# Performance work log

Hardware: AMD Instinct MI355X
Metric: run time of the kernel (lower is better)

The kernel has to match this reference:

```python
import jax, jax.numpy as jnp
from jax import lax
import numpy as np

N_ITER = 50  # entmax.EntmaxBisect default n_iter


def _p(z, alpha):
    # inverse of g'(t) = t**(alpha-1): clamp then fractional power
    return jnp.maximum(z, 0.0) ** (1.0 / (alpha - 1.0))


def entmax_bisect(x, alpha):
    """alpha-entmax over the last axis via 50-step bisection (entmax.EntmaxBisect)."""
    am1 = alpha - 1.0
    X = x * am1
    d = X.shape[-1]
    max_val = jnp.max(X, axis=-1, keepdims=True)
    tau_lo = max_val - 1.0                    # max - _gp(1, alpha)
    tau_hi = max_val - (1.0 / d) ** am1       # max - _gp(1/d, alpha)
    f_lo = jnp.sum(_p(X - tau_lo, alpha), axis=-1, keepdims=True) - 1.0
    dm0 = tau_hi - tau_lo

    def body(i, carry):
        dm, tlo, _ = carry
        dm = dm / 2.0
        tau_m = tlo + dm
        p_m = _p(X - tau_m, alpha)
        f_m = jnp.sum(p_m, axis=-1, keepdims=True) - 1.0
        mask = (f_m * f_lo) >= 0.0
        tlo = jnp.where(mask, tau_m, tlo)
        return dm, tlo, p_m

    _, _, p_m = lax.fori_loop(0, N_ITER, body, (dm0, tau_lo, jnp.zeros_like(X)))
    # ensure_sum_one=True
    return p_m / jnp.sum(p_m, axis=-1, keepdims=True)


def setup_inputs() -> dict:
    key = jax.random.key(0)
    in_value = jax.random.normal(key, (2048, 32000), dtype=jnp.float32)
    alpha = jnp.asarray(1.5, dtype=jnp.float32)  # the q parameter
    return {"in_value": in_value, "alpha": alpha}


def reference(in_value, alpha):
    return entmax_bisect(in_value, alpha)
```

## Files before the change

### kernel.cpp

```cpp
#include <hip/hip_runtime.h>
#include <math.h>


#define D_DIM   32000
#define NV4     (D_DIM / 4)
#define BLOCK   512
#define NWAVE   (BLOCK / 64)
#define NCHUNK  16
#define CAP     6144
#define NEWTON_MAX 30
#define NITER   50

__device__ __forceinline__ float wave_sum(float v) {
#pragma unroll
    for (int off = 32; off > 0; off >>= 1) v += __shfl_xor(v, off, 64);
    return v;
}
__device__ __forceinline__ float wave_max(float v) {
#pragma unroll
    for (int off = 32; off > 0; off >>= 1) v = fmaxf(v, __shfl_xor(v, off, 64));
    return v;
}
__device__ __forceinline__ float pf(float z, bool sq, float expo) {
    z = fmaxf(z, 0.0f);
    return sq ? z * z : powf(z, expo);
}
__device__ __forceinline__ unsigned fflip(float f) {
    unsigned u = __float_as_uint(f);
    return u ^ ((u >> 31) ? 0xFFFFFFFFu : 0x80000000u);
}
__device__ __forceinline__ float funflip(unsigned u) {
    return __uint_as_float(u ^ ((u & 0x80000000u) ? 0x80000000u : 0xFFFFFFFFu));
}

__global__ __launch_bounds__(BLOCK, 2)
void entmax_bisect_kernel(const float* __restrict__ x,
                          const float* __restrict__ alpha_p,
                          float* __restrict__ out) {
    const int row  = blockIdx.x;
    const int tid  = threadIdx.x;
    const int lane = tid & 63;
    const int wid  = tid >> 6;

    __shared__ float          s_val[CAP];
    __shared__ unsigned short s_idx[CAP];
    __shared__ float          s_red[NWAVE];
    __shared__ float          s_bc[2];
    __shared__ int            s_cnt;
    __shared__ unsigned       s_gmax;

    const float alpha   = alpha_p[0];
    const float am1     = alpha - 1.0f;
    const float inv_am1 = 1.0f / am1;
    const float expo    = inv_am1;
    const bool  sq      = (expo == 2.0f);

    const float4* __restrict__ x4 = (const float4*)(x + (size_t)row * D_DIM);
    float4*       __restrict__ o4 = (float4*)(out + (size_t)row * D_DIM);

    if (tid == 0) { s_cnt = 0; s_gmax = 0u; }
    __syncthreads();

    const float4 zero4 = make_float4(0.f, 0.f, 0.f, 0.f);
    float4 v[NCHUNK];
#pragma unroll
    for (int k = 0; k < NCHUNK; ++k) {
        const int i4 = tid + (k << 9);
        if (i4 < NV4) v[k] = x4[i4];
        else          v[k] = make_float4(-INFINITY, -INFINITY, -INFINITY, -INFINITY);
    }
    __builtin_amdgcn_sched_barrier(0);
#pragma unroll
    for (int k = 0; k < NCHUNK; ++k) {
        const int i4 = tid + (k << 9);
        if (i4 < NV4) o4[i4] = zero4;
    }
    __builtin_amdgcn_sched_barrier(0);

    float tm = -INFINITY;
#pragma unroll
    for (int k = 0; k < NCHUNK; ++k)
        tm = fmaxf(tm, fmaxf(fmaxf(v[k].x, v[k].y), fmaxf(v[k].z, v[k].w)));
    const float wm  = wave_max(tm);
    const float wmX = wm * am1;
    if (lane == 0) atomicMax(&s_gmax, fflip(wmX));
    const unsigned r = __hip_atomic_load(&s_gmax, __ATOMIC_RELAXED,
                                         __HIP_MEMORY_SCOPE_WORKGROUP);
    const float run   = fmaxf(funflip(r), wmX);
    const float thr_x = (run - 1.0f) * inv_am1;

    int cnt = 0;
#pragma unroll
    for (int k = 0; k < NCHUNK; ++k) {
        cnt += (v[k].x > thr_x) + (v[k].y > thr_x)
             + (v[k].z > thr_x) + (v[k].w > thr_x);
    }
    int inc = cnt;
#pragma unroll
    for (int off = 1; off < 64; off <<= 1) {
        const int t = __shfl_up(inc, off, 64);
        if (lane >= off) inc += t;
    }
    const int total = __shfl(inc, 63, 64);
    if (total > 0) {
        int base = 0;
        if (lane == 63) base = atomicAdd(&s_cnt, total);
        base = __shfl(base, 63, 64);
        int pos = base + (inc - cnt);
        auto append1 = [&](float val, int idx) {
            if (val > thr_x) {
                if (pos < CAP) {
                    s_val[pos] = val * am1;
                    s_idx[pos] = (unsigned short)idx;
                }
                ++pos;
            }
        };
#pragma unroll
        for (int k = 0; k < NCHUNK; ++k) {
            const int e = (tid << 2) + k * 2048;
            append1(v[k].x, e);     append1(v[k].y, e + 1);
            append1(v[k].z, e + 2); append1(v[k].w, e + 3);
        }
    }
    __syncthreads();
    const int   n_act   = s_cnt;
    const float max_val = funflip(s_gmax);
    const float tau_lo0 = max_val - 1.0f;

    if (n_act <= CAP) {
        if (wid == 0) {
            float tau, S;
            if (sq) {
                tau = tau_lo0;
                for (int it = 0; it < NEWTON_MAX; ++it) {
                    float s1 = 0.f, s2 = 0.f;
                    for (int i = lane; i < n_act; i += 64) {
                        const float z = fmaxf(s_val[i] - tau, 0.f);
                        s1 += z; s2 += z * z;
                    }
#pragma unroll
                    for (int off = 32; off > 0; off >>= 1) {
                        s1 += __shfl_xor(s1, off, 64);
                        s2 += __shfl_xor(s2, off, 64);
                    }
                    const float dtau = (s2 - 1.0f) / fmaxf(2.0f * s1, 1e-30f);
                    tau += dtau;
                    if (dtau < 1e-7f * fmaxf(1.0f, fabsf(tau))) break;
                }
                float s2 = 0.f;
                for (int i = lane; i < n_act; i += 64) {
                    const float z = fmaxf(s_val[i] - tau, 0.f);
                    s2 += z * z;
                }
                S = wave_sum(s2);
            } else {
                const float tau_hi = max_val - powf(1.0f / (float)D_DIM, am1);
                float dm = tau_hi - tau_lo0;
                float s = 0.f;
                for (int i = lane; i < n_act; i += 64)
                    s += pf(s_val[i] - tau_lo0, sq, expo);
                s = wave_sum(s);
                const float f_lo = s - 1.0f;
                float tlo = tau_lo0, tau_m = tau_lo0, fsum = s;
                for (int it = 0; it < NITER; ++it) {
                    dm *= 0.5f;
                    tau_m = tlo + dm;
                    float t = 0.f;
                    for (int i = lane; i < n_act; i += 64)
                        t += pf(s_val[i] - tau_m, sq, expo);
                    t = wave_sum(t);
                    fsum = t;
                    if ((t - 1.0f) * f_lo >= 0.0f) tlo = tau_m;
                }
                tau = tau_m; S = fsum;
            }
            if (lane == 0) { s_bc[0] = tau; s_bc[1] = S; }
        }
        __syncthreads();

        const float tau_f = s_bc[0];
        const float invS  = 1.0f / s_bc[1];
        for (int i = tid; i < n_act; i += BLOCK) {
            const float z = fmaxf(s_val[i] - tau_f, 0.f);
            const float p = sq ? z * z : powf(z, expo);
            out[(size_t)row * D_DIM + s_idx[i]] = p * invS;
        }
    } else {
        const float tau_hi = max_val - powf(1.0f / (float)D_DIM, am1);
        float dm = tau_hi - tau_lo0;
        float s = 0.f;
        for (int i4 = tid; i4 < NV4; i4 += BLOCK) {
            float4 vv = x4[i4];
            s += pf(vv.x * am1 - tau_lo0, sq, expo) + pf(vv.y * am1 - tau_lo0, sq, expo)
               + pf(vv.z * am1 - tau_lo0, sq, expo) + pf(vv.w * am1 - tau_lo0, sq, expo);
        }
        s = wave_sum(s);
        __syncthreads();
        if (lane == 0) s_red[wid] = s;
        __syncthreads();
        float tot = 0.f;
#pragma unroll
        for (int w = 0; w < NWAVE; ++w) tot += s_red[w];
        const float f_lo = tot - 1.0f;
        float tlo = tau_lo0, tau_m = tau_lo0, fsum = tot;
        for (int it = 0; it < NITER; ++it) {
            dm *= 0.5f;
            tau_m = tlo + dm;
            float t = 0.f;
            for (int i4 = tid; i4 < NV4; i4 += BLOCK) {
                float4 vv = x4[i4];
                t += pf(vv.x * am1 - tau_m, sq, expo) + pf(vv.y * am1 - tau_m, sq, expo)
                   + pf(vv.z * am1 - tau_m, sq, expo) + pf(vv.w * am1 - tau_m, sq, expo);
            }
            t = wave_sum(t);
            __syncthreads();
            if (lane == 0) s_red[wid] = t;
            __syncthreads();
            float tt = 0.f;
#pragma unroll
            for (int w = 0; w < NWAVE; ++w) tt += s_red[w];
            fsum = tt;
            if ((tt - 1.0f) * f_lo >= 0.0f) tlo = tau_m;
        }
        const float invS = 1.0f / fsum;
        __syncthreads();
        for (int i4 = tid; i4 < NV4; i4 += BLOCK) {
            float4 vv = x4[i4];
            float4 o;
            o.x = pf(vv.x * am1 - tau_m, sq, expo) * invS;
            o.y = pf(vv.y * am1 - tau_m, sq, expo) * invS;
            o.z = pf(vv.z * am1 - tau_m, sq, expo) * invS;
            o.w = pf(vv.w * am1 - tau_m, sq, expo) * invS;
            o4[i4] = o;
        }
    }
}

extern "C" void kernel_launch(void* const* d_in, const int* in_sizes, int n_in,
                              void* d_out, int out_size, void* d_ws, size_t ws_size,
                              hipStream_t stream) {
    const float* x       = (const float*)d_in[0];
    const float* alpha_p = (const float*)d_in[1];
    float* out           = (float*)d_out;
    const int rows       = in_sizes[0] / D_DIM;
    entmax_bisect_kernel<<<rows, BLOCK, 0, stream>>>(x, alpha_p, out);
}
```

Before: 470.5 us.

## Write dense output from registers instead of zero-fill plus sparse scatter

```diff
diff --git a/kernel.cpp b/kernel.cpp
--- a/kernel.cpp
+++ b/kernel.cpp
@@ -11,6 +11,8 @@
 #define NEWTON_MAX 30
 #define NITER   50
 
+typedef float f32x4 __attribute__((ext_vector_type(4)));
+
 __device__ __forceinline__ float wave_sum(float v) {
 #pragma unroll
     for (int off = 32; off > 0; off >>= 1) v += __shfl_xor(v, off, 64);
@@ -42,12 +44,11 @@
     const int lane = tid & 63;
     const int wid  = tid >> 6;
 
-    __shared__ float          s_val[CAP];
-    __shared__ unsigned short s_idx[CAP];
-    __shared__ float          s_red[NWAVE];
-    __shared__ float          s_bc[2];
-    __shared__ int            s_cnt;
-    __shared__ unsigned       s_gmax;
+    __shared__ float    s_val[CAP];
+    __shared__ float    s_red[NWAVE];
+    __shared__ float    s_bc[2];
+    __shared__ int      s_cnt;
+    __shared__ unsigned s_gmax;
 
     const float alpha   = alpha_p[0];
     const float am1     = alpha - 1.0f;
@@ -55,32 +56,33 @@
     const float expo    = inv_am1;
     const bool  sq      = (expo == 2.0f);
 
-    const float4* __restrict__ x4 = (const float4*)(x + (size_t)row * D_DIM);
-    float4*       __restrict__ o4 = (float4*)(out + (size_t)row * D_DIM);
+    const float* __restrict__ rowp = x + (size_t)row * D_DIM;
+    const float4* __restrict__ x4  = (const float4*)rowp;
+    float4*       __restrict__ o4  = (float4*)(out + (size_t)row * D_DIM);
 
     if (tid == 0) { s_cnt = 0; s_gmax = 0u; }
     __syncthreads();
 
-    const float4 zero4 = make_float4(0.f, 0.f, 0.f, 0.f);
-    float4 v[NCHUNK];
+    f32x4 v[NCHUNK];
 #pragma unroll
     for (int k = 0; k < NCHUNK; ++k) {
-        const int i4 = tid + (k << 9);
-        if (i4 < NV4) v[k] = x4[i4];
-        else          v[k] = make_float4(-INFINITY, -INFINITY, -INFINITY, -INFINITY);
-    }
+        const int i4   = tid + (k << 9);
+        const int safe = (i4 < NV4) ? i4 : (NV4 - 1);
+        const unsigned boff = (unsigned)safe * 16u;
+        asm volatile("global_load_dwordx4 %0, %1, %2"
+                     : "=v"(v[k]) : "v"(boff), "s"(rowp));
+    }
+    asm volatile("s_waitcnt vmcnt(0)" ::: "memory");
     __builtin_amdgcn_sched_barrier(0);
 #pragma unroll
-    for (int k = 0; k < NCHUNK; ++k) {
-        const int i4 = tid + (k << 9);
-        if (i4 < NV4) o4[i4] = zero4;
-    }
-    __builtin_amdgcn_sched_barrier(0);
+    for (int k = 0; k < NCHUNK; ++k)
+        if (tid + (k << 9) >= NV4)
+            v[k] = (f32x4){-INFINITY, -INFINITY, -INFINITY, -INFINITY};
 
     float tm = -INFINITY;
 #pragma unroll
     for (int k = 0; k < NCHUNK; ++k)
-        tm = fmaxf(tm, fmaxf(fmaxf(v[k].x, v[k].y), fmaxf(v[k].z, v[k].w)));
+        tm = fmaxf(tm, fmaxf(fmaxf(v[k][0], v[k][1]), fmaxf(v[k][2], v[k][3])));
     const float wm  = wave_max(tm);
     const float wmX = wm * am1;
     if (lane == 0) atomicMax(&s_gmax, fflip(wmX));
@@ -92,8 +94,8 @@
     int cnt = 0;
 #pragma unroll
     for (int k = 0; k < NCHUNK; ++k) {
-        cnt += (v[k].x > thr_x) + (v[k].y > thr_x)
-             + (v[k].z > thr_x) + (v[k].w > thr_x);
+        cnt += (v[k][0] > thr_x) + (v[k][1] > thr_x)
+             + (v[k][2] > thr_x) + (v[k][3] > thr_x);
     }
     int inc = cnt;
 #pragma unroll
@@ -107,20 +109,16 @@
         if (lane == 63) base = atomicAdd(&s_cnt, total);
         base = __shfl(base, 63, 64);
         int pos = base + (inc - cnt);
-        auto append1 = [&](float val, int idx) {
+        auto append1 = [&](float val) {
             if (val > thr_x) {
-                if (pos < CAP) {
-                    s_val[pos] = val * am1;
-                    s_idx[pos] = (unsigned short)idx;
-                }
+                if (pos < CAP) s_val[pos] = val * am1;
                 ++pos;
             }
         };
 #pragma unroll
         for (int k = 0; k < NCHUNK; ++k) {
-            const int e = (tid << 2) + k * 2048;
-            append1(v[k].x, e);     append1(v[k].y, e + 1);
-            append1(v[k].z, e + 2); append1(v[k].w, e + 3);
+            append1(v[k][0]); append1(v[k][1]);
+            append1(v[k][2]); append1(v[k][3]);
         }
     }
     __syncthreads();
@@ -181,10 +179,29 @@
 
         const float tau_f = s_bc[0];
         const float invS  = 1.0f / s_bc[1];
-        for (int i = tid; i < n_act; i += BLOCK) {
-            const float z = fmaxf(s_val[i] - tau_f, 0.f);
-            const float p = sq ? z * z : powf(z, expo);
-            out[(size_t)row * D_DIM + s_idx[i]] = p * invS;
+#pragma unroll
+        for (int k = 0; k < NCHUNK; ++k) {
+            const int i4 = tid + (k << 9);
+            if (i4 < NV4) {
+                float4 o;
+                {
+                    const float z = fmaxf(v[k][0] * am1 - tau_f, 0.f);
+                    o.x = (sq ? z * z : powf(z, expo)) * invS;
+                }
+                {
+                    const float z = fmaxf(v[k][1] * am1 - tau_f, 0.f);
+                    o.y = (sq ? z * z : powf(z, expo)) * invS;
+                }
+                {
+                    const float z = fmaxf(v[k][2] * am1 - tau_f, 0.f);
+                    o.z = (sq ? z * z : powf(z, expo)) * invS;
+                }
+                {
+                    const float z = fmaxf(v[k][3] * am1 - tau_f, 0.f);
+                    o.w = (sq ? z * z : powf(z, expo)) * invS;
+                }
+                o4[i4] = o;
+            }
         }
     } else {
         const float tau_hi = max_val - powf(1.0f / (float)D_DIM, am1);
@@ -224,7 +241,6 @@
             if ((tt - 1.0f) * f_lo >= 0.0f) tlo = tau_m;
         }
         const float invS = 1.0f / fsum;
-        __syncthreads();
         for (int i4 = tid; i4 < NV4; i4 += BLOCK) {
             float4 vv = x4[i4];
             float4 o;
```

Result: faster. 449.2 us (-4.5%).
